# Performance work log

Measured on AMD Instinct MI355X. Metric: run time of the kernel, lower is better.

## Reference

```python
import jax, jax.numpy as jnp
import numpy as np

E, B, L, H1, H2, C = 8, 4096, 512, 1024, 512, 40


def setup_inputs() -> dict:
    key = jax.random.key(0)
    ks = jax.random.split(key, 9)
    return {
        "x_s": jax.random.normal(ks[0], (B, L), jnp.float32),
        "x_p": jax.random.normal(ks[1], (B, L), jnp.float32),
        "W1": jax.random.normal(ks[2], (E, 2 * L, H1), jnp.float32) / np.sqrt(2 * L).astype(np.float32),
        "b1": jax.random.normal(ks[3], (E, H1), jnp.float32) * 0.01,
        "W2": jax.random.normal(ks[4], (E, H1, H2), jnp.float32) / np.sqrt(H1).astype(np.float32),
        "b2": jax.random.normal(ks[5], (E, H2), jnp.float32) * 0.01,
        "W3": jax.random.normal(ks[6], (E, H2, C), jnp.float32) / np.sqrt(H2).astype(np.float32),
        "b3": jax.random.normal(ks[7], (E, C), jnp.float32) * 0.01,
        "sub_module_label": jax.random.randint(ks[8], (B,), 0, E, dtype=jnp.int32),
        "sub_id": 0,
    }


def reference(x_s, x_p, W1, b1, W2, b2, W3, b3, sub_module_label, sub_id):
    # Encoders (EEGNet/SCN/DCN) abstracted as identity: x_s / x_p are latent features.
    # Cls_HEAD.forward: x = cat([x_p, x_s], dim=1); per-sample routed 3-layer ELU MLP head.
    # Dropout is identity in eval mode.
    x = jnp.concatenate([x_p, x_s], axis=1)                      # [B, 2L]
    h = jax.nn.elu(jnp.einsum('bi,eih->ebh', x, W1) + b1[:, None, :])   # [E, B, H1]
    h = jax.nn.elu(jnp.einsum('ebh,ehk->ebk', h, W2) + b2[:, None, :])  # [E, B, H2]
    out_all = jnp.einsum('ebk,ekc->ebc', h, W3) + b3[:, None, :]        # [E, B, C]
    # select each sample's routed expert output
    bidx = jnp.arange(x.shape[0])
    return out_all[sub_module_label, bidx]                       # [B, C]
```

## Files before the change

kernel.cpp:

```cpp
#include <hip/hip_runtime.h>
#include <hip/hip_bf16.h>
#include <math.h>

#define En   8
#define Bn   4096
#define Ln   512
#define K1n  1024
#define H1n  1024
#define H2n  512
#define Cn   40
#define NP3  48

typedef unsigned short u16;
typedef __attribute__((ext_vector_type(8))) short bf16x8;
typedef __attribute__((ext_vector_type(4))) float f32x4;

__device__ __forceinline__ u16 f2b(float f) {
    union { float f; unsigned int u; } v; v.f = f;
    unsigned int r = v.u + 0x7FFF + ((v.u >> 16) & 1);
    return (u16)(r >> 16);
}

__device__ __forceinline__ void g2l16(const void* g, void* l) {
    __builtin_amdgcn_global_load_lds(
        (const __attribute__((address_space(1))) unsigned int*)(unsigned long long)g,
        (__attribute__((address_space(3))) unsigned int*)(unsigned int)(unsigned long long)l,
        16, 0, 0);
}

__device__ __forceinline__ void wtrans64(
    const float* __restrict__ Wsrc, u16* __restrict__ Wdst,
    int K, int N, int k0, int n0, int tid, float* sm )
{
    #pragma unroll
    for (int s = 0; s < 4; s++) {
        int idx = tid + s * 256;
        int kk = idx >> 4, c4 = (idx & 15) * 4;
        float4 v = *(const float4*)&Wsrc[(size_t)(k0 + kk) * N + n0 + c4];
        float* row = sm + kk * 65 + c4;
        row[0] = v.x; row[1] = v.y; row[2] = v.z; row[3] = v.w;
    }
    __syncthreads();
    #pragma unroll
    for (int s = 0; s < 4; s++) {
        int idx = tid + s * 256;
        int nn = idx >> 4, kc = (idx & 15) * 4;
        ushort4 o = make_ushort4(f2b(sm[(kc + 0) * 65 + nn]), f2b(sm[(kc + 1) * 65 + nn]),
                                 f2b(sm[(kc + 2) * 65 + nn]), f2b(sm[(kc + 3) * 65 + nn]));
        *(ushort4*)&Wdst[(size_t)(n0 + nn) * K + k0 + kc] = o;
    }
}

#define PA_TOT 3521

__global__ __launch_bounds__(256) void prep_all(
    const float* __restrict__ xs, const float* __restrict__ xp,
    const float* __restrict__ W1, const float* __restrict__ W2,
    const float* __restrict__ W3, const float* __restrict__ b3,
    const int* __restrict__ label,
    int* __restrict__ meta, int* __restrict__ perm,
    u16* __restrict__ Xb, u16* __restrict__ W1t, u16* __restrict__ W2t,
    u16* __restrict__ W3t, float* __restrict__ outf)
{
    __shared__ __align__(16) float sm[64 * 65];
    const int bid = blockIdx.x;
    const int tid = threadIdx.x;

    if (bid == 0) {
        int* cnt = (int*)sm;
        int* off = cnt + En;
        if (tid < En) cnt[tid] = 0;
        __syncthreads();
        for (int b = tid; b < Bn; b += 256) atomicAdd(&cnt[label[b]], 1);
        __syncthreads();
        if (tid == 0) {
            int run = 0;
            for (int e = 0; e < En; e++) { off[e] = run; run += cnt[e]; }
            off[En] = run;
        }
        __syncthreads();
        if (tid < En) cnt[tid] = off[tid];
        __syncthreads();
        for (int b = tid; b < Bn; b += 256) {
            int e = label[b];
            perm[atomicAdd(&cnt[e], 1)] = b;
        }
        if (tid <= En) meta[tid] = off[tid];
    } else if (bid < 257) {
        int r0 = (bid - 1) * 16;
        #pragma unroll 4
        for (int s = 0; s < 16; s++) {
            int r = r0 + s;
            int k = tid * 4;
            const float* src = (k < Ln) ? (xp + (size_t)r * Ln + k)
                                        : (xs + (size_t)r * Ln + (k - Ln));
            float4 v = *(const float4*)src;
            *(ushort4*)&Xb[(size_t)r * K1n + k] =
                make_ushort4(f2b(v.x), f2b(v.y), f2b(v.z), f2b(v.w));
        }
    } else if (bid < 2305) {
        int b = bid - 257;
        int e = b >> 8, rem = b & 255;
        wtrans64(W1 + (size_t)e * K1n * H1n, W1t + (size_t)e * H1n * K1n,
                 K1n, H1n, (rem >> 4) * 64, (rem & 15) * 64, tid, sm);
    } else if (bid < 3329) {
        int b = bid - 2305;
        int e = b >> 7, rem = b & 127;
        wtrans64(W2 + (size_t)e * H1n * H2n, W2t + (size_t)e * H2n * H1n,
                 H1n, H2n, (rem >> 3) * 64, (rem & 7) * 64, tid, sm);
    } else if (bid < 3457) {
        int b = bid - 3329;
        int e = b >> 4, k0 = (b & 15) * 32;
        const float* src = W3 + (size_t)e * H2n * Cn;
        u16* dst = W3t + (size_t)e * NP3 * H2n;
        float* t = sm;
        #pragma unroll
        for (int q = 0; q < 5; q++) {
            int idx = tid + q * 256;
            int kk = idx / Cn, nn = idx - kk * Cn;
            if (kk < 32) t[kk * 41 + nn] = src[(size_t)(k0 + kk) * Cn + nn];
        }
        __syncthreads();
        #pragma unroll
        for (int q = 0; q < 6; q++) {
            int idx = tid + q * 256;
            int nn = idx >> 5, kk = idx & 31;
            float v = (nn < Cn) ? t[kk * 41 + nn] : 0.f;
            dst[(size_t)nn * H2n + k0 + kk] = f2b(v);
        }
    } else {
        int r0 = (bid - 3457) * 64;
        #pragma unroll
        for (int s = 0; s < 10; s++) {
            int idx = tid + s * 256;
            int r = r0 + idx / Cn;
            int c = idx - (idx / Cn) * Cn;
            outf[(size_t)r * Cn + c] = b3[label[r] * Cn + c];
        }
    }
}

template <int K, int N, int TM, int TN, bool GATHER, bool FUSE3>
__global__ __launch_bounds__(256, 2) void mfma_gemm(
    const u16* __restrict__ A, const u16* __restrict__ Wt,
    const float* __restrict__ bias, const int* __restrict__ meta,
    const int* __restrict__ perm, u16* __restrict__ outb,
    const u16* __restrict__ Wt3, float* __restrict__ outf)
{
    constexpr int BK    = 32;
    constexpr int T     = K / BK;
    constexpr int NTC   = N / TN;
    constexpr int NTRk  = Bn / TM + En;
    constexpr int NGEMM = NTRk * NTC;
    constexpr int ASLOT = TM * 4;
    constexpr int BSLOT = TN * 4;
    constexpr int STAGE = ASLOT + BSLOT;
    constexpr int ALOAD = ASLOT / 256;
    constexpr int BLOAD = BSLOT / 256;
    constexpr int LW    = ALOAD + BLOAD;
    constexpr int HSTR  = TN + 8;
    constexpr int SMST  = 4 * STAGE * 8;
    constexpr int SMU16 = (FUSE3 && (TM * HSTR) > SMST) ? (TM * HSTR) : SMST;
    __shared__ __align__(16) u16 SM[SMU16];

    const int tid = threadIdx.x;
    const int bx = blockIdx.x;

    const int gx = (bx & 7) * (NGEMM / 8) + (bx >> 3);
    const int rt = gx % NTRk;
    const int col0 = (gx / NTRk) * TN;

    int expert = -1, row0 = 0, rowmax = 0, acc_t = 0;
    int prev = meta[0];
    #pragma unroll
    for (int e = 0; e < En; e++) {
        int nxt = meta[e + 1];
        int c = nxt - prev;
        int t = (c + TM - 1) / TM;
        if (expert < 0 && rt < acc_t + t) {
            expert = e; row0 = prev + (rt - acc_t) * TM; rowmax = nxt - 1;
        }
        acc_t += t; prev = nxt;
    }
    if (expert < 0) return;

    const u16* Wexp = Wt + (size_t)expert * N * K;

    const int lane = tid & 63;
    const int wid = tid >> 6;
    const int wm = (wid & 1) * (TM / 2);
    const int wn = (wid >> 1) * (TN / 2);
    const int l15 = lane & 15;
    const int lq = lane >> 4;

    const u16* aptr[ALOAD]; int aoff[ALOAD];
    const u16* bptr[BLOAD]; int boff[BLOAD];
    #pragma unroll
    for (int s = 0; s < ALOAD; s++) {
        int idx = tid + s * 256;
        int rl = idx >> 2, c = idx & 3;
        int kq = c ^ ((rl >> 1) & 3);
        int rg = row0 + rl; if (rg > rowmax) rg = rowmax;
        if (GATHER) rg = perm[rg];
        aptr[s] = A + (size_t)rg * K + kq * 8;
        aoff[s] = idx * 8;
    }
    #pragma unroll
    for (int s = 0; s < BLOAD; s++) {
        int idx = tid + s * 256;
        int rl = idx >> 2, c = idx & 3;
        int kq = c ^ ((rl >> 1) & 3);
        bptr[s] = Wexp + (size_t)(col0 + rl) * K + kq * 8;
        boff[s] = ASLOT * 8 + idx * 8;
    }

    constexpr int MI = TM / 32;
    constexpr int NJ = TN / 32;
    f32x4 acc[MI][NJ];
    #pragma unroll
    for (int i = 0; i < MI; i++)
        #pragma unroll
        for (int j = 0; j < NJ; j++) acc[i][j] = (f32x4){0.f, 0.f, 0.f, 0.f};

    const int cp = (lq ^ ((l15 >> 1) & 3)) * 8;

    auto stage_issue = [&](int buf, int t) {
        const int base = buf * (STAGE * 8);
        const int ko = t * BK;
        #pragma unroll
        for (int s = 0; s < ALOAD; s++) g2l16(aptr[s] + ko, &SM[base + aoff[s]]);
        #pragma unroll
        for (int s = 0; s < BLOAD; s++) g2l16(bptr[s] + ko, &SM[base + boff[s]]);
    };
    auto kstep = [&](int buf) {
        const u16* As = &SM[buf * (STAGE * 8)];
        const u16* Bs = As + ASLOT * 8;
        bf16x8 af[MI], bf[NJ];
        #pragma unroll
        for (int i = 0; i < MI; i++)
            af[i] = *(const bf16x8*)&As[(wm + i * 16 + l15) * BK + cp];
        #pragma unroll
        for (int j = 0; j < NJ; j++)
            bf[j] = *(const bf16x8*)&Bs[(wn + j * 16 + l15) * BK + cp];
        #pragma unroll
        for (int i = 0; i < MI; i++)
            #pragma unroll
            for (int j = 0; j < NJ; j++)
                acc[i][j] = __builtin_amdgcn_mfma_f32_16x16x32_bf16(
                    af[i], bf[j], acc[i][j], 0, 0, 0);
    };

    stage_issue(0, 0);
    asm volatile("" ::: "memory");
    stage_issue(1, 1);
    asm volatile("" ::: "memory");
    stage_issue(2, 2);
    asm volatile("" ::: "memory");

    int rb = 0;
    for (int t = 0; t < T - 2; t++) {
        if constexpr (LW == 2)
            asm volatile("s_waitcnt vmcnt(4) lgkmcnt(0)" ::: "memory");
        else if constexpr (LW == 3)
            asm volatile("s_waitcnt vmcnt(6) lgkmcnt(0)" ::: "memory");
        else
            asm volatile("s_waitcnt vmcnt(8) lgkmcnt(0)" ::: "memory");
        __builtin_amdgcn_s_barrier();
        asm volatile("" ::: "memory");
        if (t + 3 < T) stage_issue((rb + 3) & 3, t + 3);
        asm volatile("" ::: "memory");
        kstep(rb);
        rb = (rb + 1) & 3;
    }
    if constexpr (LW == 2)
        asm volatile("s_waitcnt vmcnt(2) lgkmcnt(0)" ::: "memory");
    else if constexpr (LW == 3)
        asm volatile("s_waitcnt vmcnt(3) lgkmcnt(0)" ::: "memory");
    else
        asm volatile("s_waitcnt vmcnt(4) lgkmcnt(0)" ::: "memory");
    __builtin_amdgcn_s_barrier();
    asm volatile("" ::: "memory");
    kstep(rb);
    rb = (rb + 1) & 3;
    asm volatile("s_waitcnt vmcnt(0) lgkmcnt(0)" ::: "memory");
    __builtin_amdgcn_s_barrier();
    asm volatile("" ::: "memory");
    kstep(rb);

    if (!FUSE3) {
        #pragma unroll
        for (int i = 0; i < MI; i++) {
            #pragma unroll
            for (int j = 0; j < NJ; j++) {
                int col = col0 + wn + j * 16 + l15;
                float bv = bias[expert * N + col];
                #pragma unroll
                for (int r = 0; r < 4; r++) {
                    int grow = row0 + wm + i * 16 + lq * 4 + r;
                    if (grow <= rowmax) {
                        float v = acc[i][j][r] + bv;
                        v = (v > 0.f) ? v : (expf(v) - 1.f);
                        outb[(size_t)grow * N + col] = f2b(v);
                    }
                }
            }
        }
    } else {
        __syncthreads();
        u16* H = &SM[0];
        #pragma unroll
        for (int i = 0; i < MI; i++) {
            #pragma unroll
            for (int j = 0; j < NJ; j++) {
                int col = wn + j * 16 + l15;
                float bv = bias[expert * N + col0 + col];
                #pragma unroll
                for (int r = 0; r < 4; r++) {
                    float v = acc[i][j][r] + bv;
                    v = (v > 0.f) ? v : (expf(v) - 1.f);
                    H[(wm + i * 16 + lq * 4 + r) * HSTR + col] = f2b(v);
                }
            }
        }
        __syncthreads();
        constexpr int RI = TM / 64;
        constexpr int KC = TN / 32;
        const int rh = wid * (TM / 4);
        f32x4 a3[RI][3];
        #pragma unroll
        for (int ri = 0; ri < RI; ri++)
            #pragma unroll
            for (int j = 0; j < 3; j++) a3[ri][j] = (f32x4){0.f, 0.f, 0.f, 0.f};
        #pragma unroll
        for (int ki = 0; ki < KC; ki++) {
            bf16x8 ha[RI];
            #pragma unroll
            for (int ri = 0; ri < RI; ri++)
                ha[ri] = *(const bf16x8*)&H[(rh + ri * 16 + l15) * HSTR + ki * 32 + lq * 8];
            #pragma unroll
            for (int j = 0; j < 3; j++) {
                bf16x8 wb = *(const bf16x8*)
                    &Wt3[((size_t)expert * NP3 + j * 16 + l15) * H2n + col0 + ki * 32 + lq * 8];
                #pragma unroll
                for (int ri = 0; ri < RI; ri++)
                    a3[ri][j] = __builtin_amdgcn_mfma_f32_16x16x32_bf16(
                        ha[ri], wb, a3[ri][j], 0, 0, 0);
            }
        }
        #pragma unroll
        for (int j = 0; j < 3; j++) {
            int col = j * 16 + l15;
            if (col < Cn) {
                #pragma unroll
                for (int ri = 0; ri < RI; ri++) {
                    #pragma unroll
                    for (int r = 0; r < 4; r++) {
                        int grow = row0 + rh + ri * 16 + lq * 4 + r;
                        if (grow <= rowmax)
                            atomicAdd(&outf[(size_t)perm[grow] * Cn + col], a3[ri][j][r]);
                    }
                }
            }
        }
    }
}

extern "C" void kernel_launch(void* const* d_in, const int* in_sizes, int n_in,
                              void* d_out, int out_size, void* d_ws, size_t ws_size,
                              hipStream_t stream)
{
    const float* xs = (const float*)d_in[0];
    const float* xp = (const float*)d_in[1];
    const float* W1 = (const float*)d_in[2];
    const float* b1 = (const float*)d_in[3];
    const float* W2 = (const float*)d_in[4];
    const float* b2 = (const float*)d_in[5];
    const float* W3 = (const float*)d_in[6];
    const float* b3 = (const float*)d_in[7];
    const int* label = (const int*)d_in[8];
    float* out = (float*)d_out;

    char* ws = (char*)d_ws;
    int* meta = (int*)ws;
    int* perm = (int*)(ws + 64);
    u16* Xb  = (u16*)(ws + (64 << 10));
    u16* W1t = (u16*)(ws + (64 << 10) + (8  << 20));
    u16* W2t = (u16*)(ws + (64 << 10) + (24 << 20));
    u16* h1b = (u16*)(ws + (64 << 10) + (32 << 20));
    u16* W3t = (u16*)(ws + (64 << 10) + (40 << 20));

    prep_all<<<PA_TOT, 256, 0, stream>>>(
        xs, xp, W1, W2, W3, b3, label, meta, perm, Xb, W1t, W2t, W3t, out);

    mfma_gemm<K1n, H1n, 128, 128, true, false><<<320, 256, 0, stream>>>(
        Xb, W1t, b1, meta, perm, h1b, nullptr, out);

    mfma_gemm<H1n, H2n, 128, 128, false, true><<<160, 256, 0, stream>>>(
        h1b, W2t, b2, meta, perm, nullptr, W3t, out);
}
```

Before: 177.3 us.

## Fuse prep and both GEMMs into one cooperative persistent kernel with grid syncs

Replaces the three kernel launches with a single cooperative kernel of 640 blocks that runs phases separated by grid.sync. W2/W3 conversion and output bias init are deferred until after the first GEMM, so that work can fill idle blocks. GEMM tiles shrink (128x64 for layer 1, 64x64 for layer 2) to spread work across more blocks, and occupancy is raised to 3 blocks per CU. A three-launch fallback remains for when the cooperative launch fails. Grid-wide syncs and smaller tiles add overhead and reduce per-tile data reuse.

New measurement: 592.2 us. 3.34x slower.

```diff
diff --git a/kernel.cpp b/kernel.cpp
--- a/kernel.cpp
+++ b/kernel.cpp
@@ -1,6 +1,9 @@
 #include <hip/hip_runtime.h>
+#include <hip/hip_cooperative_groups.h>
 #include <hip/hip_bf16.h>
 #include <math.h>
+
+namespace cg = cooperative_groups;
 
 #define En   8
 #define Bn   4096
@@ -10,6 +13,7 @@
 #define H2n  512
 #define Cn   40
 #define NP3  48
+#define NB   640
 
 typedef unsigned short u16;
 typedef __attribute__((ext_vector_type(8))) short bf16x8;
@@ -49,24 +53,17 @@
                                  f2b(sm[(kc + 2) * 65 + nn]), f2b(sm[(kc + 3) * 65 + nn]));
         *(ushort4*)&Wdst[(size_t)(n0 + nn) * K + k0 + kc] = o;
     }
-}
-
-#define PA_TOT 3521
-
-__global__ __launch_bounds__(256) void prep_all(
+    __syncthreads();
+}
+
+__device__ __forceinline__ void prep1_job(
+    int j, int tid, float* sm,
     const float* __restrict__ xs, const float* __restrict__ xp,
-    const float* __restrict__ W1, const float* __restrict__ W2,
-    const float* __restrict__ W3, const float* __restrict__ b3,
-    const int* __restrict__ label,
+    const float* __restrict__ W1, const int* __restrict__ label,
     int* __restrict__ meta, int* __restrict__ perm,
-    u16* __restrict__ Xb, u16* __restrict__ W1t, u16* __restrict__ W2t,
-    u16* __restrict__ W3t, float* __restrict__ outf)
-{
-    __shared__ __align__(16) float sm[64 * 65];
-    const int bid = blockIdx.x;
-    const int tid = threadIdx.x;
-
-    if (bid == 0) {
+    u16* __restrict__ Xb, u16* __restrict__ W1t)
+{
+    if (j == 0) {
         int* cnt = (int*)sm;
         int* off = cnt + En;
         if (tid < En) cnt[tid] = 0;
@@ -86,8 +83,9 @@
             perm[atomicAdd(&cnt[e], 1)] = b;
         }
         if (tid <= En) meta[tid] = off[tid];
-    } else if (bid < 257) {
-        int r0 = (bid - 1) * 16;
+        __syncthreads();
+    } else if (j < 257) {
+        int r0 = (j - 1) * 16;
         #pragma unroll 4
         for (int s = 0; s < 16; s++) {
             int r = r0 + s;
@@ -98,18 +96,26 @@
             *(ushort4*)&Xb[(size_t)r * K1n + k] =
                 make_ushort4(f2b(v.x), f2b(v.y), f2b(v.z), f2b(v.w));
         }
-    } else if (bid < 2305) {
-        int b = bid - 257;
+    } else {
+        int b = j - 257;
         int e = b >> 8, rem = b & 255;
         wtrans64(W1 + (size_t)e * K1n * H1n, W1t + (size_t)e * H1n * K1n,
                  K1n, H1n, (rem >> 4) * 64, (rem & 15) * 64, tid, sm);
-    } else if (bid < 3329) {
-        int b = bid - 2305;
-        int e = b >> 7, rem = b & 127;
+    }
+}
+
+__device__ __forceinline__ void prep2_job(
+    int j, int tid, float* sm,
+    const float* __restrict__ W2, const float* __restrict__ W3,
+    const float* __restrict__ b3, const int* __restrict__ label,
+    u16* __restrict__ W2t, u16* __restrict__ W3t, float* __restrict__ outf)
+{
+    if (j < 1024) {
+        int e = j >> 7, rem = j & 127;
         wtrans64(W2 + (size_t)e * H1n * H2n, W2t + (size_t)e * H2n * H1n,
                  H1n, H2n, (rem >> 3) * 64, (rem & 7) * 64, tid, sm);
-    } else if (bid < 3457) {
-        int b = bid - 3329;
+    } else if (j < 1152) {
+        int b = j - 1024;
         int e = b >> 4, k0 = (b & 15) * 32;
         const float* src = W3 + (size_t)e * H2n * Cn;
         u16* dst = W3t + (size_t)e * NP3 * H2n;
@@ -128,8 +134,9 @@
             float v = (nn < Cn) ? t[kk * 41 + nn] : 0.f;
             dst[(size_t)nn * H2n + k0 + kk] = f2b(v);
         }
+        __syncthreads();
     } else {
-        int r0 = (bid - 3457) * 64;
+        int r0 = (j - 1152) * 64;
         #pragma unroll
         for (int s = 0; s < 10; s++) {
             int idx = tid + s * 256;
@@ -141,7 +148,8 @@
 }
 
 template <int K, int N, int TM, int TN, bool GATHER, bool FUSE3>
-__global__ __launch_bounds__(256, 2) void mfma_gemm(
+__device__ void gemm_body(
+    int bx, int tid, u16* SM,
     const u16* __restrict__ A, const u16* __restrict__ Wt,
     const float* __restrict__ bias, const int* __restrict__ meta,
     const int* __restrict__ perm, u16* __restrict__ outb,
@@ -159,12 +167,6 @@
     constexpr int BLOAD = BSLOT / 256;
     constexpr int LW    = ALOAD + BLOAD;
     constexpr int HSTR  = TN + 8;
-    constexpr int SMST  = 4 * STAGE * 8;
-    constexpr int SMU16 = (FUSE3 && (TM * HSTR) > SMST) ? (TM * HSTR) : SMST;
-    __shared__ __align__(16) u16 SM[SMU16];
-
-    const int tid = threadIdx.x;
-    const int bx = blockIdx.x;
 
     const int gx = (bx & 7) * (NGEMM / 8) + (bx >> 3);
     const int rt = gx % NTRk;
@@ -362,7 +364,74 @@
                 }
             }
         }
-    }
+        __syncthreads();
+    }
+}
+
+__global__ __launch_bounds__(256, 3) void fused_all(
+    const float* __restrict__ xs, const float* __restrict__ xp,
+    const float* __restrict__ W1, const float* __restrict__ b1,
+    const float* __restrict__ W2, const float* __restrict__ b2,
+    const float* __restrict__ W3, const float* __restrict__ b3,
+    const int* __restrict__ label, float* __restrict__ out,
+    int* __restrict__ meta, int* __restrict__ perm,
+    u16* __restrict__ Xb, u16* __restrict__ W1t, u16* __restrict__ W2t,
+    u16* __restrict__ h1b, u16* __restrict__ W3t)
+{
+    __shared__ __align__(16) u16 SM[24576];
+    const int bx = blockIdx.x;
+    const int tid = threadIdx.x;
+    cg::grid_group grid = cg::this_grid();
+
+    for (int j = bx; j < 2305; j += NB)
+        prep1_job(j, tid, (float*)SM, xs, xp, W1, label, meta, perm, Xb, W1t);
+
+    __threadfence();
+    grid.sync();
+    __threadfence();
+
+    gemm_body<K1n, H1n, 128, 64, true, false>(
+        bx, tid, SM, Xb, W1t, b1, meta, perm, h1b, nullptr, nullptr);
+    __syncthreads();
+    for (int j = bx; j < 1216; j += NB)
+        prep2_job(j, tid, (float*)SM, W2, W3, b3, label, W2t, W3t, out);
+
+    __threadfence();
+    grid.sync();
+    __threadfence();
+
+    if (bx < 576)
+        gemm_body<H1n, H2n, 64, 64, false, true>(
+            bx, tid, SM, h1b, W2t, b2, meta, perm, nullptr, W3t, out);
+}
+
+__global__ __launch_bounds__(256) void prep_all_fb(
+    const float* __restrict__ xs, const float* __restrict__ xp,
+    const float* __restrict__ W1, const float* __restrict__ W2,
+    const float* __restrict__ W3, const float* __restrict__ b3,
+    const int* __restrict__ label,
+    int* __restrict__ meta, int* __restrict__ perm,
+    u16* __restrict__ Xb, u16* __restrict__ W1t, u16* __restrict__ W2t,
+    u16* __restrict__ W3t, float* __restrict__ outf)
+{
+    __shared__ __align__(16) float sm[64 * 65];
+    const int bid = blockIdx.x;
+    if (bid < 2305)
+        prep1_job(bid, threadIdx.x, sm, xs, xp, W1, label, meta, perm, Xb, W1t);
+    else
+        prep2_job(bid - 2305, threadIdx.x, sm, W2, W3, b3, label, W2t, W3t, outf);
+}
+
+template <int K, int N, int TM, int TN, bool GATHER, bool FUSE3>
+__global__ __launch_bounds__(256) void gemm_fb(
+    const u16* __restrict__ A, const u16* __restrict__ Wt,
+    const float* __restrict__ bias, const int* __restrict__ meta,
+    const int* __restrict__ perm, u16* __restrict__ outb,
+    const u16* __restrict__ Wt3, float* __restrict__ outf)
+{
+    __shared__ __align__(16) u16 SM[24576];
+    gemm_body<K, N, TM, TN, GATHER, FUSE3>(
+        blockIdx.x, threadIdx.x, SM, A, Wt, bias, meta, perm, outb, Wt3, outf);
 }
 
 extern "C" void kernel_launch(void* const* d_in, const int* in_sizes, int n_in,
@@ -389,12 +458,20 @@
     u16* h1b = (u16*)(ws + (64 << 10) + (32 << 20));
     u16* W3t = (u16*)(ws + (64 << 10) + (40 << 20));
 
-    prep_all<<<PA_TOT, 256, 0, stream>>>(
-        xs, xp, W1, W2, W3, b3, label, meta, perm, Xb, W1t, W2t, W3t, out);
-
-    mfma_gemm<K1n, H1n, 128, 128, true, false><<<320, 256, 0, stream>>>(
-        Xb, W1t, b1, meta, perm, h1b, nullptr, out);
-
-    mfma_gemm<H1n, H2n, 128, 128, false, true><<<160, 256, 0, stream>>>(
-        h1b, W2t, b2, meta, perm, nullptr, W3t, out);
-}
+    void* args[] = { (void*)&xs, (void*)&xp, (void*)&W1, (void*)&b1,
+                     (void*)&W2, (void*)&b2, (void*)&W3, (void*)&b3,
+                     (void*)&label, (void*)&out, (void*)&meta, (void*)&perm,
+                     (void*)&Xb, (void*)&W1t, (void*)&W2t, (void*)&h1b,
+                     (void*)&W3t };
+    hipError_t err = hipLaunchCooperativeKernel(
+        (const void*)fused_all, dim3(NB), dim3(256), args, 0, stream);
+    if (err != hipSuccess) {
+        (void)hipGetLastError();
+        prep_all_fb<<<3521, 256, 0, stream>>>(
+            xs, xp, W1, W2, W3, b3, label, meta, perm, Xb, W1t, W2t, W3t, out);
+        gemm_fb<K1n, H1n, 128, 64, true, false><<<640, 256, 0, stream>>>(
+            Xb, W1t, b1, meta, perm, h1b, nullptr, out);
+        gemm_fb<H1n, H2n, 64, 64, false, true><<<576, 256, 0, stream>>>(
+            h1b, W2t, b2, meta, perm, nullptr, W3t, out);
+    }
+}
```
